# Kernel optimization log

Hardware: AMD Instinct MI355X
Metric: run time of the kernel (lower is better)

Reference implementation:

```python
import jax, jax.numpy as jnp
import numpy as np

INPUT_DIM = 1024
OUTPUT_DIM = 1024
DOWN = INPUT_DIM // 8  # reduction_factor=8
NUM_TOKENS = 2


def setup_inputs() -> dict:
    key = jax.random.key(0)
    k1, k2, k3, k4, k5 = jax.random.split(key, 5)
    B, Sx, Sy = 32, 2048, 512
    x = jax.random.normal(k1, (B, Sx, INPUT_DIM), dtype=jnp.float32)
    y = jax.random.normal(k2, (B, Sy, INPUT_DIM), dtype=jnp.float32)
    # nn.Parameter(torch.rand(...)) -> uniform [0,1)
    latent_tokens = jax.random.uniform(k3, (NUM_TOKENS, INPUT_DIM), dtype=jnp.float32)
    gate = jnp.zeros((1,), dtype=jnp.float32)
    # Conv1d kernel_size=1, no bias == pointwise matmul; kaiming-uniform-ish init
    lim_d = 1.0 / np.sqrt(INPUT_DIM)
    lim_u = 1.0 / np.sqrt(DOWN)
    W_down = jax.random.uniform(k4, (DOWN, INPUT_DIM), dtype=jnp.float32, minval=-lim_d, maxval=lim_d)
    W_up = jax.random.uniform(k5, (OUTPUT_DIM, DOWN), dtype=jnp.float32, minval=-lim_u, maxval=lim_u)
    return {"x": x, "y": y, "latent_tokens": latent_tokens, "gate": gate,
            "W_down": W_down, "W_up": W_up}


def reference(x, y, latent_tokens, gate, W_down, W_up):
    # tokens attend over y:  [B,T,Sy] softmax over Sy
    att_y2t = jax.nn.softmax(jnp.einsum('td,bsd->bts', latent_tokens, y), axis=-1)
    tokens = latent_tokens[None] + jnp.einsum('bts,bsd->btd', att_y2t, y)  # [B,T,D]
    # x attends over tokens: [B,Sx,T] softmax over T
    att_t2x = jax.nn.softmax(jnp.einsum('bsd,btd->bst', x, tokens), axis=-1)
    x_res = jnp.einsum('bst,btd->bsd', att_t2x, tokens)
    x = x + gate * x_res
    # 1x1 conv bottleneck: down -> ReLU -> up (pointwise matmuls)
    z = jax.nn.relu(jnp.einsum('bsd,ed->bse', x, W_down))
    out = jnp.einsum('bse,oe->bso', z, W_up)
    return out
```

## Files before the change

kernel.cpp:

```cpp
#include <hip/hip_runtime.h>
#include <hip/hip_bf16.h>

#define B_N 32
#define SX 2048
#define SY 512
#define DIM 1024
#define NTOK 2
#define DN 128
#define ODIM 1024
#define BM 64
#define BK 32
#define KSTEPS (DIM / BK)

typedef __bf16 bf16;
typedef __bf16 bf16x8 __attribute__((ext_vector_type(8)));
typedef float f32x4 __attribute__((ext_vector_type(4)));

typedef __attribute__((address_space(3))) unsigned char lds_u8;
typedef const __attribute__((address_space(1))) unsigned char glb_u8;

__device__ __forceinline__ f32x4 mfma16(bf16x8 a, bf16x8 b, f32x4 c) {
  return __builtin_amdgcn_mfma_f32_16x16x32_bf16(a, b, c, 0, 0, 0);
}

__device__ __forceinline__ void gll16(const void* g, void* l) {
  __builtin_amdgcn_global_load_lds((glb_u8*)g, (lds_u8*)l, 16, 0, 0);
}

__global__ __launch_bounds__(256) void prep_kernel(const float* __restrict__ Wd,
                                                   const float* __restrict__ Wu,
                                                   bf16* __restrict__ wdb,
                                                   bf16* __restrict__ wub) {
  int i = blockIdx.x * 256 + threadIdx.x;
  if (i < DN * DIM) {
    wdb[i] = (bf16)Wd[i];
    wub[i] = (bf16)Wu[i];
  }
}

__global__ __launch_bounds__(256) void tokens_kernel(const float* __restrict__ y,
                                                     const float* __restrict__ lat,
                                                     const float* __restrict__ gate,
                                                     float* __restrict__ tokens) {
  if (gate[0] == 0.0f) return;
  __shared__ float s_lat[NTOK][DIM];
  __shared__ float s_sc[NTOK][SY];
  int b = blockIdx.x;
  int tid = threadIdx.x, wave = tid >> 6, lane = tid & 63;
  const float* yb = y + (size_t)b * SY * DIM;
  for (int i = tid; i < NTOK * DIM; i += 256) ((float*)s_lat)[i] = lat[i];
  __syncthreads();
  for (int s = wave * 128; s < wave * 128 + 128; ++s) {
    const float* yr = yb + (size_t)s * DIM;
    float d0 = 0.f, d1 = 0.f;
#pragma unroll
    for (int i = 0; i < 4; ++i) {
      f32x4 v = *(const f32x4*)(yr + lane * 4 + i * 256);
      f32x4 l0 = *(const f32x4*)(&s_lat[0][lane * 4 + i * 256]);
      f32x4 l1 = *(const f32x4*)(&s_lat[1][lane * 4 + i * 256]);
      d0 += v[0] * l0[0] + v[1] * l0[1] + v[2] * l0[2] + v[3] * l0[3];
      d1 += v[0] * l1[0] + v[1] * l1[1] + v[2] * l1[2] + v[3] * l1[3];
    }
#pragma unroll
    for (int off = 32; off > 0; off >>= 1) {
      d0 += __shfl_xor(d0, off);
      d1 += __shfl_xor(d1, off);
    }
    if (lane == 0) { s_sc[0][s] = d0; s_sc[1][s] = d1; }
  }
  __syncthreads();
  if (wave < 2) {
    float m = -3.4e38f;
    for (int s = lane; s < SY; s += 64) m = fmaxf(m, s_sc[wave][s]);
#pragma unroll
    for (int off = 32; off > 0; off >>= 1) m = fmaxf(m, __shfl_xor(m, off));
    float sum = 0.f;
    for (int s = lane; s < SY; s += 64) {
      float e = expf(s_sc[wave][s] - m);
      s_sc[wave][s] = e;
      sum += e;
    }
#pragma unroll
    for (int off = 32; off > 0; off >>= 1) sum += __shfl_xor(sum, off);
    float inv = 1.f / sum;
    for (int s = lane; s < SY; s += 64) s_sc[wave][s] *= inv;
  }
  __syncthreads();
  float a0[4] = {0.f, 0.f, 0.f, 0.f}, a1[4] = {0.f, 0.f, 0.f, 0.f};
  for (int s = 0; s < SY; ++s) {
    float p0 = s_sc[0][s], p1 = s_sc[1][s];
    const float* yr = yb + (size_t)s * DIM;
#pragma unroll
    for (int i = 0; i < 4; ++i) {
      float v = yr[tid + i * 256];
      a0[i] += p0 * v;
      a1[i] += p1 * v;
    }
  }
  float* tb = tokens + (size_t)b * NTOK * DIM;
#pragma unroll
  for (int i = 0; i < 4; ++i) {
    tb[tid + i * 256] = s_lat[0][tid + i * 256] + a0[i];
    tb[DIM + tid + i * 256] = s_lat[1][tid + i * 256] + a1[i];
  }
}

__global__ __launch_bounds__(256) void xprime_kernel(const float* __restrict__ x,
                                                     const float* __restrict__ gate,
                                                     const float* __restrict__ tokens,
                                                     float* __restrict__ xp) {
  float g = gate[0];
  if (g == 0.0f) return;
  __shared__ float s_tok[NTOK][DIM];
  __shared__ float s_c[BM][2];
  int tid = threadIdx.x, w = tid >> 6, lane = tid & 63;
  size_t m0 = (size_t)blockIdx.x * BM;
  int b = (int)(m0 / SX);
  const float* xb = x + m0 * DIM;
  const float* tokb = tokens + (size_t)b * NTOK * DIM;
  for (int i = tid; i < NTOK * DIM; i += 256) ((float*)s_tok)[i] = tokb[i];
  __syncthreads();
  for (int i = 0; i < 16; ++i) {
    int r = w * 16 + i;
    const float* xrow = xb + (size_t)r * DIM;
    float d0 = 0.f, d1 = 0.f;
#pragma unroll
    for (int c = 0; c < 4; ++c) {
      f32x4 v = *(const f32x4*)(xrow + lane * 4 + c * 256);
      f32x4 t0 = *(const f32x4*)(&s_tok[0][lane * 4 + c * 256]);
      f32x4 t1 = *(const f32x4*)(&s_tok[1][lane * 4 + c * 256]);
      d0 += v[0] * t0[0] + v[1] * t0[1] + v[2] * t0[2] + v[3] * t0[3];
      d1 += v[0] * t1[0] + v[1] * t1[1] + v[2] * t1[2] + v[3] * t1[3];
    }
#pragma unroll
    for (int off = 32; off > 0; off >>= 1) {
      d0 += __shfl_xor(d0, off);
      d1 += __shfl_xor(d1, off);
    }
    if (lane == 0) {
      float mm = fmaxf(d0, d1);
      float e0 = expf(d0 - mm), e1 = expf(d1 - mm);
      float inv = g / (e0 + e1);
      s_c[r][0] = e0 * inv;
      s_c[r][1] = e1 * inv;
    }
  }
  __syncthreads();
  float* xpb = xp + m0 * DIM;
  for (int r = w * 16; r < w * 16 + 16; ++r) {
    float c0 = s_c[r][0], c1 = s_c[r][1];
#pragma unroll
    for (int c = 0; c < 4; ++c) {
      f32x4 v = *(const f32x4*)(xb + (size_t)r * DIM + lane * 4 + c * 256);
      f32x4 t0 = *(const f32x4*)(&s_tok[0][lane * 4 + c * 256]);
      f32x4 t1 = *(const f32x4*)(&s_tok[1][lane * 4 + c * 256]);
      f32x4 o;
#pragma unroll
      for (int j = 0; j < 4; ++j) o[j] = v[j] + c0 * t0[j] + c1 * t1[j];
      *(f32x4*)(xpb + (size_t)r * DIM + lane * 4 + c * 256) = o;
    }
  }
}

__global__ __launch_bounds__(256, 4) void main_kernel(const float* __restrict__ x,
                                                      const float* __restrict__ gate,
                                                      const float* __restrict__ xp,
                                                      const bf16* __restrict__ wdb,
                                                      const bf16* __restrict__ wub,
                                                      float* __restrict__ out) {
  __shared__ union {
    float xs[2][BM][BK];
    bf16 zs[BM * DN];
  } u;
  __shared__ bf16 ws_wd[2][DN * BK];

  int tid = threadIdx.x, w = tid >> 6, l = tid & 63;
  int lq = l >> 4, lr = l & 15;
  size_t m0 = (size_t)blockIdx.x * BM;
  float g = gate[0];
  const float* src = (g != 0.f) ? xp : x;
  const float* xb = src + m0 * DIM;

  int xrow0 = w * 8 + (l >> 3);
  int xchunk = ((l & 7) * 16) ^ (((l >> 3) & 7) << 4);
  const char* xg0 = (const char*)xb + (size_t)xrow0 * (DIM * 4) + xchunk;
  char* xl0 = (char*)&u.xs[0][0][0] + w * 1024;
  int wrow0 = w * 16 + (l >> 2);
  int wchunk = ((l & 3) * 16) ^ (((l >> 2) & 3) << 4);
  const char* wg0 = (const char*)wdb + (size_t)wrow0 * (DIM * 2) + wchunk;
  char* wl0 = (char*)ws_wd + w * 1024;

  auto STAGE = [&](int buf, int kc) {
#pragma unroll
    for (int i = 0; i < 2; ++i)
      gll16(xg0 + (size_t)i * 131072 + (size_t)kc * (BK * 4),
            xl0 + buf * 8192 + i * 4096);
#pragma unroll
    for (int i = 0; i < 2; ++i)
      gll16(wg0 + (size_t)i * 131072 + (size_t)kc * (BK * 2),
            wl0 + buf * 8192 + i * 4096);
  };

  f32x4 acc[4][2] = {};

  auto COMPUTE = [&](int buf) {
    const char* xtile = (const char*)&u.xs[buf][0][0];
    const char* wtile = (const char*)ws_wd + buf * 8192;
    bf16x8 bwf[2];
#pragma unroll
    for (int nf = 0; nf < 2; ++nf) {
      int dn = w * 32 + nf * 16 + lr;
      bwf[nf] = *(const bf16x8*)(wtile + dn * 64 + ((lq * 16) ^ ((dn & 3) << 4)));
    }
#pragma unroll
    for (int mt = 0; mt < 4; ++mt) {
      int r = mt * 16 + lr;
      f32x4 a0 = *(const f32x4*)(xtile + r * 128 + ((lq * 32) ^ ((r & 7) << 4)));
      f32x4 a1 = *(const f32x4*)(xtile + r * 128 + ((lq * 32 + 16) ^ ((r & 7) << 4)));
      bf16x8 ax;
#pragma unroll
      for (int j = 0; j < 4; ++j) { ax[j] = (bf16)a0[j]; ax[4 + j] = (bf16)a1[j]; }
      acc[mt][0] = mfma16(ax, bwf[0], acc[mt][0]);
      acc[mt][1] = mfma16(ax, bwf[1], acc[mt][1]);
    }
  };

  STAGE(0, 0);
  __syncthreads();
#pragma unroll 2
  for (int t = 0; t < KSTEPS; ++t) {
    if (t + 1 < KSTEPS) STAGE((t + 1) & 1, t + 1);
    COMPUTE(t & 1);
    __syncthreads();
  }

  char* zb = (char*)u.zs;
#pragma unroll
  for (int mt = 0; mt < 4; ++mt)
#pragma unroll
    for (int nf = 0; nf < 2; ++nf) {
      int dn = w * 32 + nf * 16 + lr;
#pragma unroll
      for (int reg = 0; reg < 4; ++reg) {
        int row = mt * 16 + lq * 4 + reg;
        float zv = fmaxf(acc[mt][nf][reg], 0.f);
        *(bf16*)(zb + row * (DN * 2) + ((2 * dn) ^ ((row & 7) << 4))) = (bf16)zv;
      }
    }
  __syncthreads();

  bf16x8 zF[4][4];
#pragma unroll
  for (int mt = 0; mt < 4; ++mt)
#pragma unroll
    for (int kkt = 0; kkt < 4; ++kkt) {
      int row = mt * 16 + lr;
      zF[mt][kkt] = *(const bf16x8*)(zb + row * (DN * 2) + ((kkt * 64 + lq * 16) ^ ((row & 7) << 4)));
    }

  float* ob = out + m0 * ODIM;
#pragma unroll 2
  for (int oc16 = 0; oc16 < 16; ++oc16) {
    int base = w * 256 + oc16 * 16;
    bf16x8 wu[4];
#pragma unroll
    for (int kkt = 0; kkt < 4; ++kkt)
      wu[kkt] = *(const bf16x8*)(wub + (size_t)(base + lr) * DN + kkt * 32 + lq * 8);
    f32x4 a2[4] = {};
#pragma unroll
    for (int kkt = 0; kkt < 4; ++kkt)
#pragma unroll
      for (int mt = 0; mt < 4; ++mt)
        a2[mt] = mfma16(wu[kkt], zF[mt][kkt], a2[mt]);
#pragma unroll
    for (int mt = 0; mt < 4; ++mt)
      *(f32x4*)(ob + (size_t)(mt * 16 + lr) * ODIM + base + lq * 4) = a2[mt];
  }
}

extern "C" void kernel_launch(void* const* d_in, const int* in_sizes, int n_in,
                              void* d_out, int out_size, void* d_ws, size_t ws_size,
                              hipStream_t stream) {
  const float* x = (const float*)d_in[0];
  const float* y = (const float*)d_in[1];
  const float* lat = (const float*)d_in[2];
  const float* gate = (const float*)d_in[3];
  const float* Wd = (const float*)d_in[4];
  const float* Wu = (const float*)d_in[5];
  float* out = (float*)d_out;
  char* ws = (char*)d_ws;

  float* tokens = (float*)ws;
  bf16* wdb = (bf16*)(ws + 262144);
  bf16* wub = (bf16*)(ws + 524288);

  prep_kernel<<<(DN * DIM + 255) / 256, 256, 0, stream>>>(Wd, Wu, wdb, wub);
  tokens_kernel<<<B_N, 256, 0, stream>>>(y, lat, gate, tokens);
  xprime_kernel<<<(B_N * SX) / BM, 256, 0, stream>>>(x, gate, tokens, out);
  main_kernel<<<(B_N * SX) / BM, 256, 0, stream>>>(x, gate, out, wdb, wub, out);
}
```

Measured before the change: 180.5 us.

## Restructure down-projection to stage bf16 x halves in LDS with 512 threads

Replaces the double-buffered global_load_lds pipeline over K=32 chunks with two large phases: each phase loads half of the 64-row x tile (512 columns), converts it to bf16 once and stores it in swizzled LDS. The W_down fragments are then read directly from global memory. The block grows to 8 waves, each owning 16 output channels of the down-projection and 128 columns of the up-projection. This removes repeated fp32-to-bf16 conversion and per-step barriers, but it loses load/compute overlap (load, sync, compute, sync) and increases per-block LDS, which may reduce occupancy.

```diff
diff --git a/kernel.cpp b/kernel.cpp
--- a/kernel.cpp
+++ b/kernel.cpp
@@ -9,22 +9,15 @@
 #define DN 128
 #define ODIM 1024
 #define BM 64
-#define BK 32
-#define KSTEPS (DIM / BK)
+#define KH 512
 
 typedef __bf16 bf16;
 typedef __bf16 bf16x8 __attribute__((ext_vector_type(8)));
+typedef __bf16 bf16x4 __attribute__((ext_vector_type(4)));
 typedef float f32x4 __attribute__((ext_vector_type(4)));
-
-typedef __attribute__((address_space(3))) unsigned char lds_u8;
-typedef const __attribute__((address_space(1))) unsigned char glb_u8;
 
 __device__ __forceinline__ f32x4 mfma16(bf16x8 a, bf16x8 b, f32x4 c) {
   return __builtin_amdgcn_mfma_f32_16x16x32_bf16(a, b, c, 0, 0, 0);
-}
-
-__device__ __forceinline__ void gll16(const void* g, void* l) {
-  __builtin_amdgcn_global_load_lds((glb_u8*)g, (lds_u8*)l, 16, 0, 0);
 }
 
 __global__ __launch_bounds__(256) void prep_kernel(const float* __restrict__ Wd,
@@ -162,116 +155,106 @@
   }
 }
 
-__global__ __launch_bounds__(256, 4) void main_kernel(const float* __restrict__ x,
+__global__ __launch_bounds__(512, 4) void main_kernel(const float* __restrict__ x,
                                                       const float* __restrict__ gate,
                                                       const float* __restrict__ xp,
                                                       const bf16* __restrict__ wdb,
                                                       const bf16* __restrict__ wub,
                                                       float* __restrict__ out) {
-  __shared__ union {
-    float xs[2][BM][BK];
-    bf16 zs[BM * DN];
-  } u;
-  __shared__ bf16 ws_wd[2][DN * BK];
-
-  int tid = threadIdx.x, w = tid >> 6, l = tid & 63;
-  int lq = l >> 4, lr = l & 15;
+  __shared__ bf16 xs[BM * KH];
+  __shared__ bf16 zsm[BM * DN];
+
+  int tid = threadIdx.x, w = tid >> 6, lane = tid & 63;
+  int lq = lane >> 4, lr = lane & 15;
   size_t m0 = (size_t)blockIdx.x * BM;
   float g = gate[0];
-  const float* src = (g != 0.f) ? xp : x;
-  const float* xb = src + m0 * DIM;
-
-  int xrow0 = w * 8 + (l >> 3);
-  int xchunk = ((l & 7) * 16) ^ (((l >> 3) & 7) << 4);
-  const char* xg0 = (const char*)xb + (size_t)xrow0 * (DIM * 4) + xchunk;
-  char* xl0 = (char*)&u.xs[0][0][0] + w * 1024;
-  int wrow0 = w * 16 + (l >> 2);
-  int wchunk = ((l & 3) * 16) ^ (((l >> 2) & 3) << 4);
-  const char* wg0 = (const char*)wdb + (size_t)wrow0 * (DIM * 2) + wchunk;
-  char* wl0 = (char*)ws_wd + w * 1024;
-
-  auto STAGE = [&](int buf, int kc) {
-#pragma unroll
-    for (int i = 0; i < 2; ++i)
-      gll16(xg0 + (size_t)i * 131072 + (size_t)kc * (BK * 4),
-            xl0 + buf * 8192 + i * 4096);
-#pragma unroll
-    for (int i = 0; i < 2; ++i)
-      gll16(wg0 + (size_t)i * 131072 + (size_t)kc * (BK * 2),
-            wl0 + buf * 8192 + i * 4096);
+  const float* xb = ((g != 0.f) ? xp : x) + m0 * DIM;
+
+  char* xls = (char*)xs;
+  char* zls = (char*)zsm;
+
+  f32x4 acc[4] = {};
+
+  auto LOADH = [&](int h) {
+    f32x4 xv[8][2];
+#pragma unroll
+    for (int i = 0; i < 8; ++i) {
+      int row = w + i * 8;
+      const float* p = xb + (size_t)row * DIM + h * KH + lane * 8;
+      xv[i][0] = *(const f32x4*)p;
+      xv[i][1] = *(const f32x4*)(p + 4);
+    }
+#pragma unroll
+    for (int i = 0; i < 8; ++i) {
+      int row = w + i * 8;
+      bf16x8 o;
+#pragma unroll
+      for (int j = 0; j < 4; ++j) {
+        o[j] = (bf16)xv[i][0][j];
+        o[4 + j] = (bf16)xv[i][1][j];
+      }
+      *(bf16x8*)(xls + row * (KH * 2) + ((lane * 16) ^ (w << 4))) = o;
+    }
   };
 
-  f32x4 acc[4][2] = {};
-
-  auto COMPUTE = [&](int buf) {
-    const char* xtile = (const char*)&u.xs[buf][0][0];
-    const char* wtile = (const char*)ws_wd + buf * 8192;
-    bf16x8 bwf[2];
-#pragma unroll
-    for (int nf = 0; nf < 2; ++nf) {
-      int dn = w * 32 + nf * 16 + lr;
-      bwf[nf] = *(const bf16x8*)(wtile + dn * 64 + ((lq * 16) ^ ((dn & 3) << 4)));
-    }
-#pragma unroll
-    for (int mt = 0; mt < 4; ++mt) {
-      int r = mt * 16 + lr;
-      f32x4 a0 = *(const f32x4*)(xtile + r * 128 + ((lq * 32) ^ ((r & 7) << 4)));
-      f32x4 a1 = *(const f32x4*)(xtile + r * 128 + ((lq * 32 + 16) ^ ((r & 7) << 4)));
-      bf16x8 ax;
-#pragma unroll
-      for (int j = 0; j < 4; ++j) { ax[j] = (bf16)a0[j]; ax[4 + j] = (bf16)a1[j]; }
-      acc[mt][0] = mfma16(ax, bwf[0], acc[mt][0]);
-      acc[mt][1] = mfma16(ax, bwf[1], acc[mt][1]);
+  auto COMPH = [&](int h) {
+    const bf16* wdw = wdb + (size_t)(w * 16 + lr) * DIM + h * KH + lq * 8;
+#pragma unroll 4
+    for (int kc = 0; kc < KH / 32; ++kc) {
+      bf16x8 wf = *(const bf16x8*)(wdw + kc * 32);
+#pragma unroll
+      for (int mt = 0; mt < 4; ++mt) {
+        int xr = mt * 16 + lr;
+        bf16x8 xf = *(const bf16x8*)(xls + xr * (KH * 2) +
+                                     (((kc * 32 + lq * 8) * 2) ^ ((xr & 7) << 4)));
+        acc[mt] = mfma16(wf, xf, acc[mt]);
+      }
     }
   };
 
-  STAGE(0, 0);
-  __syncthreads();
-#pragma unroll 2
-  for (int t = 0; t < KSTEPS; ++t) {
-    if (t + 1 < KSTEPS) STAGE((t + 1) & 1, t + 1);
-    COMPUTE(t & 1);
-    __syncthreads();
-  }
-
-  char* zb = (char*)u.zs;
+  LOADH(0);
+  __syncthreads();
+  COMPH(0);
+  __syncthreads();
+  LOADH(1);
+  __syncthreads();
+  COMPH(1);
+
+#pragma unroll
+  for (int mt = 0; mt < 4; ++mt) {
+    int xr = mt * 16 + lr;
+    int dn = w * 16 + lq * 4;
+    bf16x4 pk;
+#pragma unroll
+    for (int r = 0; r < 4; ++r) pk[r] = (bf16)fmaxf(acc[mt][r], 0.f);
+    *(bf16x4*)(zls + xr * (DN * 2) + ((dn * 2) ^ ((xr & 7) << 4))) = pk;
+  }
+  __syncthreads();
+
+  bf16x8 zF[4][4];
 #pragma unroll
   for (int mt = 0; mt < 4; ++mt)
 #pragma unroll
-    for (int nf = 0; nf < 2; ++nf) {
-      int dn = w * 32 + nf * 16 + lr;
-#pragma unroll
-      for (int reg = 0; reg < 4; ++reg) {
-        int row = mt * 16 + lq * 4 + reg;
-        float zv = fmaxf(acc[mt][nf][reg], 0.f);
-        *(bf16*)(zb + row * (DN * 2) + ((2 * dn) ^ ((row & 7) << 4))) = (bf16)zv;
-      }
-    }
-  __syncthreads();
-
-  bf16x8 zF[4][4];
-#pragma unroll
-  for (int mt = 0; mt < 4; ++mt)
-#pragma unroll
-    for (int kkt = 0; kkt < 4; ++kkt) {
-      int row = mt * 16 + lr;
-      zF[mt][kkt] = *(const bf16x8*)(zb + row * (DN * 2) + ((kkt * 64 + lq * 16) ^ ((row & 7) << 4)));
+    for (int kt = 0; kt < 4; ++kt) {
+      int xr = mt * 16 + lr;
+      zF[kt][mt] = *(const bf16x8*)(zls + xr * (DN * 2) +
+                                    (((kt * 32 + lq * 8) * 2) ^ ((xr & 7) << 4)));
     }
 
   float* ob = out + m0 * ODIM;
 #pragma unroll 2
-  for (int oc16 = 0; oc16 < 16; ++oc16) {
-    int base = w * 256 + oc16 * 16;
+  for (int oc16 = 0; oc16 < 8; ++oc16) {
+    int base = w * 128 + oc16 * 16;
     bf16x8 wu[4];
 #pragma unroll
-    for (int kkt = 0; kkt < 4; ++kkt)
-      wu[kkt] = *(const bf16x8*)(wub + (size_t)(base + lr) * DN + kkt * 32 + lq * 8);
+    for (int kt = 0; kt < 4; ++kt)
+      wu[kt] = *(const bf16x8*)(wub + (size_t)(base + lr) * DN + kt * 32 + lq * 8);
     f32x4 a2[4] = {};
 #pragma unroll
-    for (int kkt = 0; kkt < 4; ++kkt)
+    for (int kt = 0; kt < 4; ++kt)
 #pragma unroll
       for (int mt = 0; mt < 4; ++mt)
-        a2[mt] = mfma16(wu[kkt], zF[mt][kkt], a2[mt]);
+        a2[mt] = mfma16(wu[kt], zF[kt][mt], a2[mt]);
 #pragma unroll
     for (int mt = 0; mt < 4; ++mt)
       *(f32x4*)(ob + (size_t)(mt * 16 + lr) * ODIM + base + lq * 4) = a2[mt];
@@ -297,5 +280,5 @@
   prep_kernel<<<(DN * DIM + 255) / 256, 256, 0, stream>>>(Wd, Wu, wdb, wub);
   tokens_kernel<<<B_N, 256, 0, stream>>>(y, lat, gate, tokens);
   xprime_kernel<<<(B_N * SX) / BM, 256, 0, stream>>>(x, gate, tokens, out);
-  main_kernel<<<(B_N * SX) / BM, 256, 0, stream>>>(x, gate, out, wdb, wub, out);
-}
+  main_kernel<<<(B_N * SX) / BM, 512, 0, stream>>>(x, gate, out, wdb, wub, out);
+}
```

After: 162.6 us. 1.11x faster.
